# Performance work log

Measured on AMD Instinct MI355X. Metric: run time of the kernel, lower is better.

Reference implementation:

```python
import jax, jax.numpy as jnp
import numpy as np

N_NODES = 100000
IN_F = 128
HID = 64
NUM_CLS = 16
N_EDGES = 1600000
NEG_SLOPE = 0.2


def setup_inputs() -> dict:
    key = jax.random.key(0)
    ks = jax.random.split(key, 10)
    x = jax.random.normal(ks[0], (N_NODES, IN_F), dtype=jnp.float32)
    edge_index = jax.random.randint(ks[1], (2, N_EDGES), 0, N_NODES, dtype=jnp.int64)
    s1 = 1.0 / np.sqrt(IN_F)
    s2 = 1.0 / np.sqrt(HID)
    W1 = jax.random.normal(ks[2], (IN_F, HID), dtype=jnp.float32) * s1
    att_src1 = jax.random.normal(ks[3], (HID,), dtype=jnp.float32) * s2
    att_dst1 = jax.random.normal(ks[4], (HID,), dtype=jnp.float32) * s2
    b1 = jnp.zeros((HID,), dtype=jnp.float32)
    W2 = jax.random.normal(ks[5], (HID, NUM_CLS), dtype=jnp.float32) * s2
    att_src2 = jax.random.normal(ks[6], (NUM_CLS,), dtype=jnp.float32) * 0.25
    att_dst2 = jax.random.normal(ks[7], (NUM_CLS,), dtype=jnp.float32) * 0.25
    b2 = jnp.zeros((NUM_CLS,), dtype=jnp.float32)
    return {"x": x, "edge_index": edge_index, "W1": W1, "att_src1": att_src1,
            "att_dst1": att_dst1, "b1": b1, "W2": W2, "att_src2": att_src2,
            "att_dst2": att_dst2, "b2": b2}


def _gat_conv(x, src, dst, W, a_src, a_dst, b, n_nodes):
    # PyG GATConv, heads=1: h = xW; e_ij = LeakyReLU(a_src.h_j + a_dst.h_i)
    h = x @ W  # [N, D]
    e_s = h @ a_src  # [N]
    e_d = h @ a_dst  # [N]
    e = jax.nn.leaky_relu(e_s[src] + e_d[dst], NEG_SLOPE)  # [E]
    # segment softmax over incoming edges per destination node
    m = jax.ops.segment_max(e, dst, num_segments=n_nodes)  # [N]
    ex = jnp.exp(e - m[dst])
    z = jax.ops.segment_sum(ex, dst, num_segments=n_nodes)  # [N]
    alpha = ex / z[dst]  # [E]
    out = jax.ops.segment_sum(h[src] * alpha[:, None], dst, num_segments=n_nodes)
    return out + b


def reference(x, edge_index, W1, att_src1, att_dst1, b1, W2, att_src2, att_dst2, b2):
    n = x.shape[0]
    # add_self_loops=True (PyG default): guarantees non-empty neighborhoods
    loops = jnp.arange(n, dtype=edge_index.dtype)
    src = jnp.concatenate([edge_index[0], loops])
    dst = jnp.concatenate([edge_index[1], loops])
    h = _gat_conv(x, src, dst, W1, att_src1, att_dst1, b1, n)
    h = jax.nn.relu(h)
    # dropout is identity in eval mode
    out = _gat_conv(h, src, dst, W2, att_src2, att_dst2, b2, n)
    return jax.nn.log_softmax(out, axis=1)
```

## Files before the change

### kernel.cpp

```cpp
#include <hip/hip_runtime.h>

#define NEG_SLOPE 0.2f
#define LOG2E 1.44269504f
#define NBUCK 1024
#define BCAP 2560
#define EPB_MAX 8192
#define DCAP 96

typedef __attribute__((ext_vector_type(8))) short bf16x8;
typedef __attribute__((ext_vector_type(4))) float f32x4;

static __device__ __forceinline__ float lrelu(float x) { return fmaxf(x, NEG_SLOPE * x); }

static __device__ __forceinline__ float b2f(unsigned short u) {
    union { unsigned int i; float f; } c; c.i = ((unsigned int)u) << 16; return c.f;
}
static __device__ __forceinline__ unsigned short f2b(float f) {
    union { float f; unsigned int i; } c; c.f = f;
    unsigned int r = c.i + 0x7fff + ((c.i >> 16) & 1);
    return (unsigned short)(r >> 16);
}


__global__ __launch_bounds__(256) void bucket_place(const int* __restrict__ src, const int* __restrict__ dst,
                                                    unsigned int* __restrict__ gblock, int* __restrict__ blkofs,
                                                    int ne, int epb) {
    __shared__ int cnt[NBUCK];
    __shared__ unsigned int stage[EPB_MAX];
    __shared__ int ws4[4];
    __shared__ int totals;
    int tid = threadIdx.x, lane = tid & 63, wid = tid >> 6;
    int blk = blockIdx.x;
    for (int i = tid; i < NBUCK; i += 256) cnt[i] = 0;
    __syncthreads();
    int lo = blk * epb;
    int hi = min(ne, lo + epb);
    for (int i = lo + tid; i < hi; i += 256) atomicAdd(&cnt[dst[i] >> 7], 1);
    __syncthreads();
    int c0 = cnt[4 * tid + 0], c1 = cnt[4 * tid + 1], c2 = cnt[4 * tid + 2], c3 = cnt[4 * tid + 3];
    int s = c0 + c1 + c2 + c3;
    int incl = s;
    #pragma unroll
    for (int off = 1; off < 64; off <<= 1) {
        int u = __shfl_up(incl, off, 64);
        if (lane >= off) incl += u;
    }
    if (lane == 63) ws4[wid] = incl;
    __syncthreads();
    if (tid < 4) {
        int v = ws4[tid];
        int iv = v;
        #pragma unroll
        for (int off = 1; off < 4; off <<= 1) {
            int u = __shfl_up(iv, off, 64);
            if (tid >= off) iv += u;
        }
        ws4[tid] = iv;
        if (tid == 3) totals = iv;
    }
    __syncthreads();
    int base = incl - s + (wid > 0 ? ws4[wid - 1] : 0);
    long long brow = (long long)blk * (NBUCK + 1);
    int o0 = base, o1 = base + c0, o2 = base + c0 + c1, o3 = base + c0 + c1 + c2;
    blkofs[brow + 4 * tid + 0] = o0;
    blkofs[brow + 4 * tid + 1] = o1;
    blkofs[brow + 4 * tid + 2] = o2;
    blkofs[brow + 4 * tid + 3] = o3;
    __syncthreads();
    cnt[4 * tid + 0] = o0; cnt[4 * tid + 1] = o1;
    cnt[4 * tid + 2] = o2; cnt[4 * tid + 3] = o3;
    if (tid == 255) blkofs[brow + NBUCK] = totals;
    __syncthreads();
    for (int i = lo + tid; i < hi; i += 256) {
        int d = dst[i];
        int p = atomicAdd(&cnt[d >> 7], 1);
        stage[p] = (unsigned int)src[i] | (((unsigned int)(d & 127)) << 17);
    }
    __syncthreads();
    int total = totals;
    for (int i = tid; i < total; i += 256)
        gblock[(size_t)blk * epb + i] = stage[i];
}


__global__ __launch_bounds__(256) void bucket_csr(const unsigned int* __restrict__ gblock,
                                                  const int* __restrict__ blkofs,
                                                  int* __restrict__ rowstart, int* __restrict__ deg,
                                                  int* __restrict__ csrc, int n, int epb) {
    int b = blockIdx.x;
    int nodebase = b << 7;
    if (nodebase >= n) return;
    __shared__ unsigned int stage[BCAP];
    __shared__ int hist[128], cur[128], ws[4];
    __shared__ int totals;
    int tid = threadIdx.x, lane = tid & 63, wid = tid >> 6;
    long long brow = (long long)tid * (NBUCK + 1);
    int r0 = blkofs[brow + b];
    int r1 = blkofs[brow + b + 1];
    int len = r1 - r0;
    int incl = len;
    #pragma unroll
    for (int off = 1; off < 64; off <<= 1) {
        int u = __shfl_up(incl, off, 64);
        if (lane >= off) incl += u;
    }
    if (lane == 63) ws[wid] = incl;
    __syncthreads();
    if (tid < 4) {
        int v = ws[tid];
        int iv = v;
        #pragma unroll
        for (int off = 1; off < 4; off <<= 1) {
            int u = __shfl_up(iv, off, 64);
            if (tid >= off) iv += u;
        }
        ws[tid] = iv;
        if (tid == 3) totals = iv;
    }
    __syncthreads();
    int myofs = incl - len + (wid > 0 ? ws[wid - 1] : 0);
    for (int k = 0; k < len; ++k) {
        int p = myofs + k;
        if (p < BCAP) stage[p] = gblock[(size_t)tid * epb + r0 + k];
    }
    if (tid < 128) hist[tid] = 0;
    __syncthreads();
    int cntb = min(totals, BCAP);
    for (int i = tid; i < cntb; i += 256) atomicAdd(&hist[(stage[i] >> 17) & 127], 1);
    __syncthreads();
    int v = 0, incl2 = 0;
    if (tid < 128) {
        v = hist[tid];
        incl2 = v;
        #pragma unroll
        for (int off = 1; off < 64; off <<= 1) {
            int u = __shfl_up(incl2, off, 64);
            if (lane >= off) incl2 += u;
        }
        if (lane == 63) ws[wid] = incl2;
    }
    __syncthreads();
    if (tid < 128) {
        int excl = incl2 - v + (wid == 1 ? ws[0] : 0);
        int node = nodebase + tid;
        if (node < n) { rowstart[node] = b * BCAP + excl; deg[node] = v; }
        cur[tid] = excl;
    }
    __syncthreads();
    for (int i = tid; i < cntb; i += 256) {
        unsigned int e = stage[i];
        int ld = (e >> 17) & 127;
        int p = atomicAdd(&cur[ld], 1);
        csrc[b * BCAP + p] = (int)(e & 0x1FFFFu);
    }
}


__global__ __launch_bounds__(256) void wprep(const float* __restrict__ W1,
                                             unsigned short* __restrict__ WfH,
                                             unsigned short* __restrict__ WfL) {
    int lane = threadIdx.x & 63, cb = threadIdx.x >> 6;
    int r16 = lane & 15, g4 = lane >> 4;
    for (int kb = 0; kb < 4; ++kb) {
        #pragma unroll
        for (int i = 0; i < 8; ++i) {
            int k = kb * 32 + g4 * 8 + i;
            float v = W1[k * 64 + cb * 16 + r16];
            unsigned short hi = f2b(v);
            unsigned short lo = f2b(v - b2f(hi));
            WfH[((cb * 4 + kb) * 64 + lane) * 8 + i] = hi;
            WfL[((cb * 4 + kb) * 64 + lane) * 8 + i] = lo;
        }
    }
}


__global__ __launch_bounds__(256) void gemm1(const float* __restrict__ x,
                                             const unsigned short* __restrict__ WfH,
                                             const unsigned short* __restrict__ WfL,
                                             const float* __restrict__ asrc, const float* __restrict__ adst,
                                             unsigned short* __restrict__ h, float* __restrict__ es,
                                             float* __restrict__ ed, int n) {
    __shared__ unsigned short AsH[64 * 128];
    __shared__ unsigned short AsL[64 * 128];
    int tid = threadIdx.x, lane = tid & 63, wid = tid >> 6;
    int r16 = lane & 15, g4 = lane >> 4;

    int base = blockIdx.x * 64;
    #pragma unroll
    for (int jj = 0; jj < 8; ++jj) {
        int idx = tid + jj * 256;
        int r = idx >> 5, c4 = idx & 31;
        int nidx = base + r;
        float4 v = make_float4(0.f, 0.f, 0.f, 0.f);
        if (nidx < n) v = *(const float4*)&x[(size_t)nidx * 128 + c4 * 4];
        unsigned short h0 = f2b(v.x), h1_ = f2b(v.y), h2_ = f2b(v.z), h3_ = f2b(v.w);
        unsigned short l0 = f2b(v.x - b2f(h0)), l1 = f2b(v.y - b2f(h1_));
        unsigned short l2 = f2b(v.z - b2f(h2_)), l3 = f2b(v.w - b2f(h3_));
        int u = c4 >> 1;
        int swz = (((u ^ (r & 15)) << 1) | (c4 & 1)) << 2;
        *(unsigned long long*)&AsH[r * 128 + swz] =
            (unsigned long long)h0 | ((unsigned long long)h1_ << 16) |
            ((unsigned long long)h2_ << 32) | ((unsigned long long)h3_ << 48);
        *(unsigned long long*)&AsL[r * 128 + swz] =
            (unsigned long long)l0 | ((unsigned long long)l1 << 16) |
            ((unsigned long long)l2 << 32) | ((unsigned long long)l3 << 48);
    }
    __syncthreads();

    bf16x8 afH[4], afL[4];
    int arow = wid * 16 + r16;
    #pragma unroll
    for (int kb = 0; kb < 4; ++kb) {
        int uu = (kb * 4 + g4) ^ r16;
        afH[kb] = *(const bf16x8*)&AsH[arow * 128 + uu * 8];
        afL[kb] = *(const bf16x8*)&AsL[arow * 128 + uu * 8];
    }

    f32x4 acc[4] = {{0.f,0.f,0.f,0.f},{0.f,0.f,0.f,0.f},{0.f,0.f,0.f,0.f},{0.f,0.f,0.f,0.f}};
    #pragma unroll
    for (int cb = 0; cb < 4; ++cb) {
        #pragma unroll
        for (int kb = 0; kb < 4; ++kb) {
            bf16x8 bH = *(const bf16x8*)&WfH[((cb * 4 + kb) * 64 + lane) * 8];
            bf16x8 bL = *(const bf16x8*)&WfL[((cb * 4 + kb) * 64 + lane) * 8];
            acc[cb] = __builtin_amdgcn_mfma_f32_16x16x32_bf16(afH[kb], bH, acc[cb], 0, 0, 0);
            acc[cb] = __builtin_amdgcn_mfma_f32_16x16x32_bf16(afL[kb], bH, acc[cb], 0, 0, 0);
            acc[cb] = __builtin_amdgcn_mfma_f32_16x16x32_bf16(afH[kb], bL, acc[cb], 0, 0, 0);
        }
    }

    float ps[4] = {0.f,0.f,0.f,0.f}, pd[4] = {0.f,0.f,0.f,0.f};
    #pragma unroll
    for (int cb = 0; cb < 4; ++cb) {
        int col = cb * 16 + r16;
        float av = asrc[col], dv = adst[col];
        #pragma unroll
        for (int rg = 0; rg < 4; ++rg) {
            int nidx = base + wid * 16 + g4 * 4 + rg;
            float v = acc[cb][rg];
            if (nidx < n) h[(size_t)nidx * 64 + col] = f2b(v);
            ps[rg] = fmaf(v, av, ps[rg]);
            pd[rg] = fmaf(v, dv, pd[rg]);
        }
    }
    #pragma unroll
    for (int off = 8; off >= 1; off >>= 1) {
        #pragma unroll
        for (int rg = 0; rg < 4; ++rg) {
            ps[rg] += __shfl_xor(ps[rg], off, 64);
            pd[rg] += __shfl_xor(pd[rg], off, 64);
        }
    }
    if (r16 == 0) {
        #pragma unroll
        for (int rg = 0; rg < 4; ++rg) {
            int nidx = base + wid * 16 + g4 * 4 + rg;
            if (nidx < n) { es[nidx] = ps[rg] * LOG2E; ed[nidx] = pd[rg] * LOG2E; }
        }
    }
}


static __device__ __forceinline__ void prep_phase(const float* __restrict__ es, const float* __restrict__ ed,
                                                  const int* __restrict__ rowstart, const int* __restrict__ deg,
                                                  const int* __restrict__ csrc,
                                                  float2 (*ealds)[DCAP], float* aselfs,
                                                  int node, int ln, int l32) {
    float edn = ed[node];
    float e0 = lrelu(es[node] + edn);
    int s0 = rowstart[node], cnt = min(deg[node], DCAP);
    int padded = (cnt + 7) & ~7;
    if (cnt <= 32) {
        int sl = 0; float e = -3.0e38f;
        if (l32 < cnt) { sl = csrc[s0 + l32]; e = lrelu(es[sl] + edn); }
        float m = fmaxf(e, e0);
        #pragma unroll
        for (int off = 16; off >= 1; off >>= 1) m = fmaxf(m, __shfl_xor(m, off, 64));
        float p = (l32 < cnt) ? __builtin_amdgcn_exp2f(e - m) : 0.f;
        float z = p;
        #pragma unroll
        for (int off = 16; off >= 1; off >>= 1) z += __shfl_xor(z, off, 64);
        float p0 = __builtin_amdgcn_exp2f(e0 - m);
        float zi = 1.f / (z + p0);
        if (l32 < cnt) ealds[ln][l32] = make_float2(__int_as_float(sl), p * zi);
        else if (l32 < padded) ealds[ln][l32] = make_float2(__int_as_float(node), 0.f);
        if (l32 == 0) aselfs[ln] = p0 * zi;
    } else {
        float m = e0;
        for (int c = l32; c < cnt; c += 32)
            m = fmaxf(m, lrelu(es[csrc[s0 + c]] + edn));
        #pragma unroll
        for (int off = 16; off >= 1; off >>= 1) m = fmaxf(m, __shfl_xor(m, off, 64));
        float z = 0.f;
        for (int c = l32; c < cnt; c += 32) {
            int sl = csrc[s0 + c];
            float p = __builtin_amdgcn_exp2f(lrelu(es[sl] + edn) - m);
            ealds[ln][c] = make_float2(__int_as_float(sl), p);
            z += p;
        }
        #pragma unroll
        for (int off = 16; off >= 1; off >>= 1) z += __shfl_xor(z, off, 64);
        float p0 = __builtin_amdgcn_exp2f(e0 - m);
        float zi = 1.f / (z + p0);
        for (int c = l32; c < cnt; c += 32) ealds[ln][c].y *= zi;
        if (l32 < padded - cnt) ealds[ln][cnt + l32] = make_float2(__int_as_float(node), 0.f);
        if (l32 == 0) aselfs[ln] = p0 * zi;
    }
}


__global__ __launch_bounds__(256) void fgather1(const unsigned short* __restrict__ h,
                                                const float* __restrict__ es, const float* __restrict__ ed,
                                                const float* __restrict__ b1,
                                                const int* __restrict__ rowstart, const int* __restrict__ deg,
                                                const int* __restrict__ csrc,
                                                unsigned short* __restrict__ out, int n) {
    __shared__ float2 ealds[8][DCAP];
    __shared__ float aselfs[8];
    int wid = threadIdx.x >> 6, lane = threadIdx.x & 63;
    int half = lane >> 5, l32 = lane & 31;
    int nbase = blockIdx.x * 8;
    int pnode = nbase + wid * 2 + half;
    if (pnode < n)
        prep_phase(es, ed, rowstart, deg, csrc, ealds, aselfs, pnode, wid * 2 + half, l32);
    __syncthreads();

    int sg = lane >> 4, q = lane & 15;
    for (int t = 0; t < 2; ++t) {
        int node = nbase + wid * 2 + t;
        if (node >= n) break;
        int ln = wid * 2 + t;
        float a0_, a1_, a2_, a3_;
        {
            ushort4 hv = *(const ushort4*)&h[(unsigned)(node * 64) + q * 4];
            float a = (sg == 0) ? aselfs[ln] : 0.f;
            a0_ = a * b2f(hv.x); a1_ = a * b2f(hv.y);
            a2_ = a * b2f(hv.z); a3_ = a * b2f(hv.w);
        }
        int cnt = min(deg[node], DCAP);
        int iters = (cnt + 3) >> 2;
        int j = 0;
        for (; j + 4 <= iters; j += 4) {
            float2 tA = ealds[ln][(j + 0) * 4 + sg];
            float2 tB = ealds[ln][(j + 1) * 4 + sg];
            float2 tC = ealds[ln][(j + 2) * 4 + sg];
            float2 tD = ealds[ln][(j + 3) * 4 + sg];
            int sA = __float_as_int(tA.x), sB = __float_as_int(tB.x);
            int sC = __float_as_int(tC.x), sD = __float_as_int(tD.x);
            ushort4 hA = *(const ushort4*)&h[(unsigned)(sA * 64) + q * 4];
            ushort4 hB = *(const ushort4*)&h[(unsigned)(sB * 64) + q * 4];
            ushort4 hC = *(const ushort4*)&h[(unsigned)(sC * 64) + q * 4];
            ushort4 hD = *(const ushort4*)&h[(unsigned)(sD * 64) + q * 4];
            a0_ = fmaf(b2f(hA.x), tA.y, a0_); a1_ = fmaf(b2f(hA.y), tA.y, a1_);
            a2_ = fmaf(b2f(hA.z), tA.y, a2_); a3_ = fmaf(b2f(hA.w), tA.y, a3_);
            a0_ = fmaf(b2f(hB.x), tB.y, a0_); a1_ = fmaf(b2f(hB.y), tB.y, a1_);
            a2_ = fmaf(b2f(hB.z), tB.y, a2_); a3_ = fmaf(b2f(hB.w), tB.y, a3_);
            a0_ = fmaf(b2f(hC.x), tC.y, a0_); a1_ = fmaf(b2f(hC.y), tC.y, a1_);
            a2_ = fmaf(b2f(hC.z), tC.y, a2_); a3_ = fmaf(b2f(hC.w), tC.y, a3_);
            a0_ = fmaf(b2f(hD.x), tD.y, a0_); a1_ = fmaf(b2f(hD.y), tD.y, a1_);
            a2_ = fmaf(b2f(hD.z), tD.y, a2_); a3_ = fmaf(b2f(hD.w), tD.y, a3_);
        }
        for (; j < iters; ++j) {
            float2 tE = ealds[ln][j * 4 + sg];
            int s = __float_as_int(tE.x);
            ushort4 hv = *(const ushort4*)&h[(unsigned)(s * 64) + q * 4];
            a0_ = fmaf(b2f(hv.x), tE.y, a0_); a1_ = fmaf(b2f(hv.y), tE.y, a1_);
            a2_ = fmaf(b2f(hv.z), tE.y, a2_); a3_ = fmaf(b2f(hv.w), tE.y, a3_);
        }
        #pragma unroll
        for (int off = 16; off <= 32; off <<= 1) {
            a0_ += __shfl_xor(a0_, off, 64);
            a1_ += __shfl_xor(a1_, off, 64);
            a2_ += __shfl_xor(a2_, off, 64);
            a3_ += __shfl_xor(a3_, off, 64);
        }
        if (sg == 0) {
            float o0 = a0_ + b1[q * 4 + 0], o1 = a1_ + b1[q * 4 + 1];
            float o2 = a2_ + b1[q * 4 + 2], o3 = a3_ + b1[q * 4 + 3];
            ushort4 pk;
            pk.x = f2b(o0 > 0.f ? o0 : 0.f); pk.y = f2b(o1 > 0.f ? o1 : 0.f);
            pk.z = f2b(o2 > 0.f ? o2 : 0.f); pk.w = f2b(o3 > 0.f ? o3 : 0.f);
            *(ushort4*)&out[(unsigned)(node * 64) + q * 4] = pk;
        }
    }
}


__global__ __launch_bounds__(256) void gemm2(const unsigned short* __restrict__ hin, const float* __restrict__ W2,
                                             const float* __restrict__ asrc, const float* __restrict__ adst,
                                             unsigned short* __restrict__ h2, float* __restrict__ es,
                                             float* __restrict__ ed, int n) {
    __shared__ float xl[16][64];
    int tid = threadIdx.x;
    int lane = tid & 63, wid = tid >> 6;
    int sub = lane >> 4, j = lane & 15;
    float w2[64];
    #pragma unroll
    for (int k = 0; k < 64; ++k) w2[k] = W2[k * 16 + j];
    int base = blockIdx.x * 16;
    for (int i = tid; i < 16 * 64; i += 256) {
        int r = i >> 6, c = i & 63;
        int nidx = base + r;
        xl[r][c] = (nidx < n) ? b2f(hin[(unsigned)(nidx * 64) + c]) : 0.f;
    }
    __syncthreads();
    int r = wid * 4 + sub;
    int nidx = base + r;
    if (nidx < n) {
        float acc = 0.f;
        #pragma unroll
        for (int kk = 0; kk < 16; ++kk) {
            float4 xv = *(const float4*)&xl[r][kk * 4];
            acc = fmaf(xv.x, w2[4 * kk + 0], acc);
            acc = fmaf(xv.y, w2[4 * kk + 1], acc);
            acc = fmaf(xv.z, w2[4 * kk + 2], acc);
            acc = fmaf(xv.w, w2[4 * kk + 3], acc);
        }
        h2[(unsigned)(nidx * 16) + j] = f2b(acc);
        float s = acc * asrc[j], d = acc * adst[j];
        #pragma unroll
        for (int off = 8; off >= 1; off >>= 1) {
            s += __shfl_xor(s, off, 64);
            d += __shfl_xor(d, off, 64);
        }
        if (j == 0) { es[nidx] = s * LOG2E; ed[nidx] = d * LOG2E; }
    }
}


__global__ __launch_bounds__(256) void fgather2(const unsigned short* __restrict__ h,
                                                const float* __restrict__ es, const float* __restrict__ ed,
                                                const float* __restrict__ b2,
                                                const int* __restrict__ rowstart, const int* __restrict__ deg,
                                                const int* __restrict__ csrc,
                                                float* __restrict__ out, int n) {
    __shared__ float2 ealds[8][DCAP];
    __shared__ float aselfs[8];
    int wid = threadIdx.x >> 6, lane = threadIdx.x & 63;
    int half = lane >> 5, l32 = lane & 31;
    int nbase = blockIdx.x * 8;
    int pnode = nbase + wid * 2 + half;
    if (pnode < n)
        prep_phase(es, ed, rowstart, deg, csrc, ealds, aselfs, pnode, wid * 2 + half, l32);
    __syncthreads();

    int sg = lane >> 3, p = lane & 7;
    for (int t = 0; t < 2; ++t) {
        int node = nbase + wid * 2 + t;
        if (node >= n) break;
        int ln = wid * 2 + t;
        float a0_, a1_;
        {
            ushort2 hv = *(const ushort2*)&h[(unsigned)(node * 16) + p * 2];
            float a = (sg == 0) ? aselfs[ln] : 0.f;
            a0_ = a * b2f(hv.x); a1_ = a * b2f(hv.y);
        }
        int cnt = min(deg[node], DCAP);
        int iters = (cnt + 7) >> 3;
        int j = 0;
        for (; j + 2 <= iters; j += 2) {
            float2 tA = ealds[ln][(j + 0) * 8 + sg];
            float2 tB = ealds[ln][(j + 1) * 8 + sg];
            int sA = __float_as_int(tA.x), sB = __float_as_int(tB.x);
            ushort2 hA = *(const ushort2*)&h[(unsigned)(sA * 16) + p * 2];
            ushort2 hB = *(const ushort2*)&h[(unsigned)(sB * 16) + p * 2];
            a0_ = fmaf(b2f(hA.x), tA.y, a0_); a1_ = fmaf(b2f(hA.y), tA.y, a1_);
            a0_ = fmaf(b2f(hB.x), tB.y, a0_); a1_ = fmaf(b2f(hB.y), tB.y, a1_);
        }
        for (; j < iters; ++j) {
            float2 tE = ealds[ln][j * 8 + sg];
            int s = __float_as_int(tE.x);
            ushort2 hv = *(const ushort2*)&h[(unsigned)(s * 16) + p * 2];
            a0_ = fmaf(b2f(hv.x), tE.y, a0_); a1_ = fmaf(b2f(hv.y), tE.y, a1_);
        }
        #pragma unroll
        for (int off = 8; off <= 32; off <<= 1) {
            a0_ += __shfl_xor(a0_, off, 64);
            a1_ += __shfl_xor(a1_, off, 64);
        }
        float v0 = a0_ + b2[p * 2 + 0];
        float v1 = a1_ + b2[p * 2 + 1];
        float mx = fmaxf(v0, v1);
        #pragma unroll
        for (int off = 4; off >= 1; off >>= 1) mx = fmaxf(mx, __shfl_xor(mx, off, 64));
        float se = __expf(v0 - mx) + __expf(v1 - mx);
        #pragma unroll
        for (int off = 4; off >= 1; off >>= 1) se += __shfl_xor(se, off, 64);
        float ls = __logf(se);
        if (sg == 0) {
            float2 res = make_float2(v0 - mx - ls, v1 - mx - ls);
            *(float2*)&out[(unsigned)(node * 16) + p * 2] = res;
        }
    }
}


extern "C" void kernel_launch(void* const* d_in, const int* in_sizes, int n_in,
                              void* d_out, int out_size, void* d_ws, size_t ws_size,
                              hipStream_t stream) {
    const float* x   = (const float*)d_in[0];
    const int*   ei  = (const int*)d_in[1];
    const float* W1  = (const float*)d_in[2];
    const float* as1 = (const float*)d_in[3];
    const float* ad1 = (const float*)d_in[4];
    const float* b1  = (const float*)d_in[5];
    const float* W2  = (const float*)d_in[6];
    const float* as2 = (const float*)d_in[7];
    const float* ad2 = (const float*)d_in[8];
    const float* b2  = (const float*)d_in[9];
    int n  = in_sizes[0] / 128;
    int ne = in_sizes[1] / 2;
    const int* srcv = ei;
    const int* dstv = ei + ne;

    char* ws = (char*)d_ws;
    size_t off = 0;
    auto alloc = [&](size_t bytes) -> void* {
        void* p = ws + off;
        off = (off + bytes + 255) & ~(size_t)255;
        return p;
    };
    unsigned short* h1 = (unsigned short*)alloc((size_t)n * 64 * 2);
    unsigned short* hr = (unsigned short*)alloc((size_t)n * 64 * 2);
    unsigned short* h2 = (unsigned short*)alloc((size_t)n * 16 * 2);
    float* es1  = (float*)alloc((size_t)n * 4);
    float* ed1  = (float*)alloc((size_t)n * 4);
    float* es2  = (float*)alloc((size_t)n * 4);
    float* ed2  = (float*)alloc((size_t)n * 4);
    unsigned short* WfH = (unsigned short*)alloc(16 * 64 * 8 * 2);
    unsigned short* WfL = (unsigned short*)alloc(16 * 64 * 8 * 2);
    int* deg      = (int*)alloc((size_t)n * 4);
    int* rowstart = (int*)alloc((size_t)n * 4);
    int nblk = 256;
    int epb = (ne + nblk - 1) / nblk;
    unsigned int* gblock = (unsigned int*)alloc((size_t)nblk * epb * 4);
    int* blkofs   = (int*)alloc((size_t)nblk * (NBUCK + 1) * 4);
    int* csrc     = (int*)alloc((size_t)NBUCK * BCAP * 4);

    bucket_place<<<nblk, 256, 0, stream>>>(srcv, dstv, gblock, blkofs, ne, epb);
    bucket_csr<<<NBUCK, 256, 0, stream>>>(gblock, blkofs, rowstart, deg, csrc, n, epb);

    wprep<<<1, 256, 0, stream>>>(W1, WfH, WfL);
    gemm1<<<(n + 63) / 64, 256, 0, stream>>>(x, WfH, WfL, as1, ad1, h1, es1, ed1, n);
    fgather1<<<(n + 7) / 8, 256, 0, stream>>>(h1, es1, ed1, b1, rowstart, deg, csrc, hr, n);

    gemm2<<<(n + 15) / 16, 256, 0, stream>>>(hr, W2, as2, ad2, h2, es2, ed2, n);
    fgather2<<<(n + 7) / 8, 256, 0, stream>>>(h2, es2, ed2, b2, rowstart, deg, csrc, (float*)d_out, n);
}
```

Measured before the change: 170.0 us.

## Merge bucket placement and first GEMM into one heterogeneous launch

```diff
diff --git a/kernel.cpp b/kernel.cpp
--- a/kernel.cpp
+++ b/kernel.cpp
@@ -22,64 +22,156 @@
 }
 
 
-__global__ __launch_bounds__(256) void bucket_place(const int* __restrict__ src, const int* __restrict__ dst,
-                                                    unsigned int* __restrict__ gblock, int* __restrict__ blkofs,
-                                                    int ne, int epb) {
-    __shared__ int cnt[NBUCK];
-    __shared__ unsigned int stage[EPB_MAX];
+__global__ __launch_bounds__(256) void k1(const int* __restrict__ src, const int* __restrict__ dst,
+                                          unsigned int* __restrict__ gblock, int* __restrict__ blkofs,
+                                          int ne, int epb, int nplace,
+                                          const float* __restrict__ x, const float* __restrict__ W1,
+                                          const float* __restrict__ asrc, const float* __restrict__ adst,
+                                          unsigned short* __restrict__ h, float* __restrict__ es,
+                                          float* __restrict__ ed, int n) {
+    __shared__ __align__(16) char smem[4096 + EPB_MAX * 4];
     __shared__ int ws4[4];
     __shared__ int totals;
     int tid = threadIdx.x, lane = tid & 63, wid = tid >> 6;
-    int blk = blockIdx.x;
-    for (int i = tid; i < NBUCK; i += 256) cnt[i] = 0;
-    __syncthreads();
-    int lo = blk * epb;
-    int hi = min(ne, lo + epb);
-    for (int i = lo + tid; i < hi; i += 256) atomicAdd(&cnt[dst[i] >> 7], 1);
-    __syncthreads();
-    int c0 = cnt[4 * tid + 0], c1 = cnt[4 * tid + 1], c2 = cnt[4 * tid + 2], c3 = cnt[4 * tid + 3];
-    int s = c0 + c1 + c2 + c3;
-    int incl = s;
-    #pragma unroll
-    for (int off = 1; off < 64; off <<= 1) {
-        int u = __shfl_up(incl, off, 64);
-        if (lane >= off) incl += u;
-    }
-    if (lane == 63) ws4[wid] = incl;
-    __syncthreads();
-    if (tid < 4) {
-        int v = ws4[tid];
-        int iv = v;
-        #pragma unroll
-        for (int off = 1; off < 4; off <<= 1) {
-            int u = __shfl_up(iv, off, 64);
-            if (tid >= off) iv += u;
-        }
-        ws4[tid] = iv;
-        if (tid == 3) totals = iv;
-    }
-    __syncthreads();
-    int base = incl - s + (wid > 0 ? ws4[wid - 1] : 0);
-    long long brow = (long long)blk * (NBUCK + 1);
-    int o0 = base, o1 = base + c0, o2 = base + c0 + c1, o3 = base + c0 + c1 + c2;
-    blkofs[brow + 4 * tid + 0] = o0;
-    blkofs[brow + 4 * tid + 1] = o1;
-    blkofs[brow + 4 * tid + 2] = o2;
-    blkofs[brow + 4 * tid + 3] = o3;
-    __syncthreads();
-    cnt[4 * tid + 0] = o0; cnt[4 * tid + 1] = o1;
-    cnt[4 * tid + 2] = o2; cnt[4 * tid + 3] = o3;
-    if (tid == 255) blkofs[brow + NBUCK] = totals;
-    __syncthreads();
-    for (int i = lo + tid; i < hi; i += 256) {
-        int d = dst[i];
-        int p = atomicAdd(&cnt[d >> 7], 1);
-        stage[p] = (unsigned int)src[i] | (((unsigned int)(d & 127)) << 17);
-    }
-    __syncthreads();
-    int total = totals;
-    for (int i = tid; i < total; i += 256)
-        gblock[(size_t)blk * epb + i] = stage[i];
+
+    if (blockIdx.x < (unsigned)nplace) {
+        int* cnt = (int*)smem;
+        unsigned int* stage = (unsigned int*)(smem + 4096);
+        int blk = blockIdx.x;
+        for (int i = tid; i < NBUCK; i += 256) cnt[i] = 0;
+        __syncthreads();
+        int lo = blk * epb;
+        int hi = min(ne, lo + epb);
+        for (int i = lo + tid; i < hi; i += 256) atomicAdd(&cnt[dst[i] >> 7], 1);
+        __syncthreads();
+        int c0 = cnt[4 * tid + 0], c1 = cnt[4 * tid + 1], c2 = cnt[4 * tid + 2], c3 = cnt[4 * tid + 3];
+        int s = c0 + c1 + c2 + c3;
+        int incl = s;
+        #pragma unroll
+        for (int off = 1; off < 64; off <<= 1) {
+            int u = __shfl_up(incl, off, 64);
+            if (lane >= off) incl += u;
+        }
+        if (lane == 63) ws4[wid] = incl;
+        __syncthreads();
+        if (tid < 4) {
+            int v = ws4[tid];
+            int iv = v;
+            #pragma unroll
+            for (int off = 1; off < 4; off <<= 1) {
+                int u = __shfl_up(iv, off, 64);
+                if (tid >= off) iv += u;
+            }
+            ws4[tid] = iv;
+            if (tid == 3) totals = iv;
+        }
+        __syncthreads();
+        int base = incl - s + (wid > 0 ? ws4[wid - 1] : 0);
+        long long brow = (long long)blk * (NBUCK + 1);
+        int o0 = base, o1 = base + c0, o2 = base + c0 + c1, o3 = base + c0 + c1 + c2;
+        blkofs[brow + 4 * tid + 0] = o0;
+        blkofs[brow + 4 * tid + 1] = o1;
+        blkofs[brow + 4 * tid + 2] = o2;
+        blkofs[brow + 4 * tid + 3] = o3;
+        __syncthreads();
+        cnt[4 * tid + 0] = o0; cnt[4 * tid + 1] = o1;
+        cnt[4 * tid + 2] = o2; cnt[4 * tid + 3] = o3;
+        if (tid == 255) blkofs[brow + NBUCK] = totals;
+        __syncthreads();
+        for (int i = lo + tid; i < hi; i += 256) {
+            int d = dst[i];
+            int p = atomicAdd(&cnt[d >> 7], 1);
+            stage[p] = (unsigned int)src[i] | (((unsigned int)(d & 127)) << 17);
+        }
+        __syncthreads();
+        int total = totals;
+        for (int i = tid; i < total; i += 256)
+            gblock[(size_t)blk * epb + i] = stage[i];
+    } else {
+        unsigned short* AsH = (unsigned short*)smem;
+        unsigned short* AsL = (unsigned short*)(smem + 16384);
+        int r16 = lane & 15, g4 = lane >> 4;
+        int base = (blockIdx.x - nplace) * 64;
+        #pragma unroll
+        for (int jj = 0; jj < 8; ++jj) {
+            int idx = tid + jj * 256;
+            int r = idx >> 5, c4 = idx & 31;
+            int nidx = base + r;
+            float4 v = make_float4(0.f, 0.f, 0.f, 0.f);
+            if (nidx < n) v = *(const float4*)&x[(size_t)nidx * 128 + c4 * 4];
+            unsigned short h0 = f2b(v.x), h1_ = f2b(v.y), h2_ = f2b(v.z), h3_ = f2b(v.w);
+            unsigned short l0 = f2b(v.x - b2f(h0)), l1 = f2b(v.y - b2f(h1_));
+            unsigned short l2 = f2b(v.z - b2f(h2_)), l3 = f2b(v.w - b2f(h3_));
+            int u = c4 >> 1;
+            int swz = (((u ^ (r & 15)) << 1) | (c4 & 1)) << 2;
+            *(unsigned long long*)&AsH[r * 128 + swz] =
+                (unsigned long long)h0 | ((unsigned long long)h1_ << 16) |
+                ((unsigned long long)h2_ << 32) | ((unsigned long long)h3_ << 48);
+            *(unsigned long long*)&AsL[r * 128 + swz] =
+                (unsigned long long)l0 | ((unsigned long long)l1 << 16) |
+                ((unsigned long long)l2 << 32) | ((unsigned long long)l3 << 48);
+        }
+        __syncthreads();
+
+        bf16x8 afH[4], afL[4];
+        int arow = wid * 16 + r16;
+        #pragma unroll
+        for (int kb = 0; kb < 4; ++kb) {
+            int uu = (kb * 4 + g4) ^ r16;
+            afH[kb] = *(const bf16x8*)&AsH[arow * 128 + uu * 8];
+            afL[kb] = *(const bf16x8*)&AsL[arow * 128 + uu * 8];
+        }
+
+        f32x4 acc[4] = {{0.f,0.f,0.f,0.f},{0.f,0.f,0.f,0.f},{0.f,0.f,0.f,0.f},{0.f,0.f,0.f,0.f}};
+        #pragma unroll
+        for (int cb = 0; cb < 4; ++cb) {
+            #pragma unroll
+            for (int kb = 0; kb < 4; ++kb) {
+                union { bf16x8 v; unsigned short u[8]; } bH, bL;
+                #pragma unroll
+                for (int i = 0; i < 8; ++i) {
+                    int k = kb * 32 + g4 * 8 + i;
+                    float w = W1[k * 64 + cb * 16 + r16];
+                    unsigned short hi = f2b(w);
+                    bH.u[i] = hi;
+                    bL.u[i] = f2b(w - b2f(hi));
+                }
+                acc[cb] = __builtin_amdgcn_mfma_f32_16x16x32_bf16(afH[kb], bH.v, acc[cb], 0, 0, 0);
+                acc[cb] = __builtin_amdgcn_mfma_f32_16x16x32_bf16(afL[kb], bH.v, acc[cb], 0, 0, 0);
+                acc[cb] = __builtin_amdgcn_mfma_f32_16x16x32_bf16(afH[kb], bL.v, acc[cb], 0, 0, 0);
+            }
+        }
+
+        float ps[4] = {0.f,0.f,0.f,0.f}, pd[4] = {0.f,0.f,0.f,0.f};
+        #pragma unroll
+        for (int cb = 0; cb < 4; ++cb) {
+            int col = cb * 16 + r16;
+            float av = asrc[col], dv = adst[col];
+            #pragma unroll
+            for (int rg = 0; rg < 4; ++rg) {
+                int nidx = base + wid * 16 + g4 * 4 + rg;
+                float v = acc[cb][rg];
+                if (nidx < n) h[(size_t)nidx * 64 + col] = f2b(v);
+                ps[rg] = fmaf(v, av, ps[rg]);
+                pd[rg] = fmaf(v, dv, pd[rg]);
+            }
+        }
+        #pragma unroll
+        for (int off = 8; off >= 1; off >>= 1) {
+            #pragma unroll
+            for (int rg = 0; rg < 4; ++rg) {
+                ps[rg] += __shfl_xor(ps[rg], off, 64);
+                pd[rg] += __shfl_xor(pd[rg], off, 64);
+            }
+        }
+        if (r16 == 0) {
+            #pragma unroll
+            for (int rg = 0; rg < 4; ++rg) {
+                int nidx = base + wid * 16 + g4 * 4 + rg;
+                if (nidx < n) { es[nidx] = ps[rg] * LOG2E; ed[nidx] = pd[rg] * LOG2E; }
+            }
+        }
+    }
 }
 
 
@@ -152,112 +244,6 @@
         int ld = (e >> 17) & 127;
         int p = atomicAdd(&cur[ld], 1);
         csrc[b * BCAP + p] = (int)(e & 0x1FFFFu);
-    }
-}
-
-
-__global__ __launch_bounds__(256) void wprep(const float* __restrict__ W1,
-                                             unsigned short* __restrict__ WfH,
-                                             unsigned short* __restrict__ WfL) {
-    int lane = threadIdx.x & 63, cb = threadIdx.x >> 6;
-    int r16 = lane & 15, g4 = lane >> 4;
-    for (int kb = 0; kb < 4; ++kb) {
-        #pragma unroll
-        for (int i = 0; i < 8; ++i) {
-            int k = kb * 32 + g4 * 8 + i;
-            float v = W1[k * 64 + cb * 16 + r16];
-            unsigned short hi = f2b(v);
-            unsigned short lo = f2b(v - b2f(hi));
-            WfH[((cb * 4 + kb) * 64 + lane) * 8 + i] = hi;
-            WfL[((cb * 4 + kb) * 64 + lane) * 8 + i] = lo;
-        }
-    }
-}
-
-
-__global__ __launch_bounds__(256) void gemm1(const float* __restrict__ x,
-                                             const unsigned short* __restrict__ WfH,
-                                             const unsigned short* __restrict__ WfL,
-                                             const float* __restrict__ asrc, const float* __restrict__ adst,
-                                             unsigned short* __restrict__ h, float* __restrict__ es,
-                                             float* __restrict__ ed, int n) {
-    __shared__ unsigned short AsH[64 * 128];
-    __shared__ unsigned short AsL[64 * 128];
-    int tid = threadIdx.x, lane = tid & 63, wid = tid >> 6;
-    int r16 = lane & 15, g4 = lane >> 4;
-
-    int base = blockIdx.x * 64;
-    #pragma unroll
-    for (int jj = 0; jj < 8; ++jj) {
-        int idx = tid + jj * 256;
-        int r = idx >> 5, c4 = idx & 31;
-        int nidx = base + r;
-        float4 v = make_float4(0.f, 0.f, 0.f, 0.f);
-        if (nidx < n) v = *(const float4*)&x[(size_t)nidx * 128 + c4 * 4];
-        unsigned short h0 = f2b(v.x), h1_ = f2b(v.y), h2_ = f2b(v.z), h3_ = f2b(v.w);
-        unsigned short l0 = f2b(v.x - b2f(h0)), l1 = f2b(v.y - b2f(h1_));
-        unsigned short l2 = f2b(v.z - b2f(h2_)), l3 = f2b(v.w - b2f(h3_));
-        int u = c4 >> 1;
-        int swz = (((u ^ (r & 15)) << 1) | (c4 & 1)) << 2;
-        *(unsigned long long*)&AsH[r * 128 + swz] =
-            (unsigned long long)h0 | ((unsigned long long)h1_ << 16) |
-            ((unsigned long long)h2_ << 32) | ((unsigned long long)h3_ << 48);
-        *(unsigned long long*)&AsL[r * 128 + swz] =
-            (unsigned long long)l0 | ((unsigned long long)l1 << 16) |
-            ((unsigned long long)l2 << 32) | ((unsigned long long)l3 << 48);
-    }
-    __syncthreads();
-
-    bf16x8 afH[4], afL[4];
-    int arow = wid * 16 + r16;
-    #pragma unroll
-    for (int kb = 0; kb < 4; ++kb) {
-        int uu = (kb * 4 + g4) ^ r16;
-        afH[kb] = *(const bf16x8*)&AsH[arow * 128 + uu * 8];
-        afL[kb] = *(const bf16x8*)&AsL[arow * 128 + uu * 8];
-    }
-
-    f32x4 acc[4] = {{0.f,0.f,0.f,0.f},{0.f,0.f,0.f,0.f},{0.f,0.f,0.f,0.f},{0.f,0.f,0.f,0.f}};
-    #pragma unroll
-    for (int cb = 0; cb < 4; ++cb) {
-        #pragma unroll
-        for (int kb = 0; kb < 4; ++kb) {
-            bf16x8 bH = *(const bf16x8*)&WfH[((cb * 4 + kb) * 64 + lane) * 8];
-            bf16x8 bL = *(const bf16x8*)&WfL[((cb * 4 + kb) * 64 + lane) * 8];
-            acc[cb] = __builtin_amdgcn_mfma_f32_16x16x32_bf16(afH[kb], bH, acc[cb], 0, 0, 0);
-            acc[cb] = __builtin_amdgcn_mfma_f32_16x16x32_bf16(afL[kb], bH, acc[cb], 0, 0, 0);
-            acc[cb] = __builtin_amdgcn_mfma_f32_16x16x32_bf16(afH[kb], bL, acc[cb], 0, 0, 0);
-        }
-    }
-
-    float ps[4] = {0.f,0.f,0.f,0.f}, pd[4] = {0.f,0.f,0.f,0.f};
-    #pragma unroll
-    for (int cb = 0; cb < 4; ++cb) {
-        int col = cb * 16 + r16;
-        float av = asrc[col], dv = adst[col];
-        #pragma unroll
-        for (int rg = 0; rg < 4; ++rg) {
-            int nidx = base + wid * 16 + g4 * 4 + rg;
-            float v = acc[cb][rg];
-            if (nidx < n) h[(size_t)nidx * 64 + col] = f2b(v);
-            ps[rg] = fmaf(v, av, ps[rg]);
-            pd[rg] = fmaf(v, dv, pd[rg]);
-        }
-    }
-    #pragma unroll
-    for (int off = 8; off >= 1; off >>= 1) {
-        #pragma unroll
-        for (int rg = 0; rg < 4; ++rg) {
-            ps[rg] += __shfl_xor(ps[rg], off, 64);
-            pd[rg] += __shfl_xor(pd[rg], off, 64);
-        }
-    }
-    if (r16 == 0) {
-        #pragma unroll
-        for (int rg = 0; rg < 4; ++rg) {
-            int nidx = base + wid * 16 + g4 * 4 + rg;
-            if (nidx < n) { es[nidx] = ps[rg] * LOG2E; ed[nidx] = pd[rg] * LOG2E; }
-        }
     }
 }
 
@@ -528,23 +514,19 @@
     float* ed1  = (float*)alloc((size_t)n * 4);
     float* es2  = (float*)alloc((size_t)n * 4);
     float* ed2  = (float*)alloc((size_t)n * 4);
-    unsigned short* WfH = (unsigned short*)alloc(16 * 64 * 8 * 2);
-    unsigned short* WfL = (unsigned short*)alloc(16 * 64 * 8 * 2);
     int* deg      = (int*)alloc((size_t)n * 4);
     int* rowstart = (int*)alloc((size_t)n * 4);
-    int nblk = 256;
-    int epb = (ne + nblk - 1) / nblk;
-    unsigned int* gblock = (unsigned int*)alloc((size_t)nblk * epb * 4);
-    int* blkofs   = (int*)alloc((size_t)nblk * (NBUCK + 1) * 4);
+    int nplace = 256;
+    int epb = (ne + nplace - 1) / nplace;
+    unsigned int* gblock = (unsigned int*)alloc((size_t)nplace * epb * 4);
+    int* blkofs   = (int*)alloc((size_t)nplace * (NBUCK + 1) * 4);
     int* csrc     = (int*)alloc((size_t)NBUCK * BCAP * 4);
 
-    bucket_place<<<nblk, 256, 0, stream>>>(srcv, dstv, gblock, blkofs, ne, epb);
+    int ngemm = (n + 63) / 64;
+    k1<<<nplace + ngemm, 256, 0, stream>>>(srcv, dstv, gblock, blkofs, ne, epb, nplace,
+                                           x, W1, as1, ad1, h1, es1, ed1, n);
     bucket_csr<<<NBUCK, 256, 0, stream>>>(gblock, blkofs, rowstart, deg, csrc, n, epb);
-
-    wprep<<<1, 256, 0, stream>>>(W1, WfH, WfL);
-    gemm1<<<(n + 63) / 64, 256, 0, stream>>>(x, WfH, WfL, as1, ad1, h1, es1, ed1, n);
     fgather1<<<(n + 7) / 8, 256, 0, stream>>>(h1, es1, ed1, b1, rowstart, deg, csrc, hr, n);
-
     gemm2<<<(n + 15) / 16, 256, 0, stream>>>(hr, W2, as2, ad2, h2, es2, ed2, n);
     fgather2<<<(n + 7) / 8, 256, 0, stream>>>(h2, es2, ed2, b2, rowstart, deg, csrc, (float*)d_out, n);
 }
```

New measurement: 149.4 us, median of 3. -12.2%, faster.

## Merge bucket placement and first GEMM into one launch for concurrent execution

Applied to the files above, without the earlier changes.

```diff
diff --git a/kernel.cpp b/kernel.cpp
--- a/kernel.cpp
+++ b/kernel.cpp
@@ -22,64 +22,170 @@
 }
 
 
-__global__ __launch_bounds__(256) void bucket_place(const int* __restrict__ src, const int* __restrict__ dst,
-                                                    unsigned int* __restrict__ gblock, int* __restrict__ blkofs,
-                                                    int ne, int epb) {
-    __shared__ int cnt[NBUCK];
-    __shared__ unsigned int stage[EPB_MAX];
+__global__ __launch_bounds__(256) void wprep(const float* __restrict__ W1,
+                                             unsigned short* __restrict__ WfH,
+                                             unsigned short* __restrict__ WfL) {
+    int lane = threadIdx.x & 63, cb = threadIdx.x >> 6;
+    int r16 = lane & 15, g4 = lane >> 4;
+    for (int kb = 0; kb < 4; ++kb) {
+        #pragma unroll
+        for (int i = 0; i < 8; ++i) {
+            int k = kb * 32 + g4 * 8 + i;
+            float v = W1[k * 64 + cb * 16 + r16];
+            unsigned short hi = f2b(v);
+            unsigned short lo = f2b(v - b2f(hi));
+            WfH[((cb * 4 + kb) * 64 + lane) * 8 + i] = hi;
+            WfL[((cb * 4 + kb) * 64 + lane) * 8 + i] = lo;
+        }
+    }
+}
+
+
+__global__ __launch_bounds__(256) void k1(const int* __restrict__ src, const int* __restrict__ dst,
+                                          unsigned int* __restrict__ gblock, int* __restrict__ blkofs,
+                                          int ne, int epb, int nplace,
+                                          const float* __restrict__ x,
+                                          const unsigned short* __restrict__ WfH,
+                                          const unsigned short* __restrict__ WfL,
+                                          const float* __restrict__ asrc, const float* __restrict__ adst,
+                                          unsigned short* __restrict__ h, float* __restrict__ es,
+                                          float* __restrict__ ed, int n) {
+    __shared__ __align__(16) char smem[4096 + EPB_MAX * 4];
     __shared__ int ws4[4];
     __shared__ int totals;
     int tid = threadIdx.x, lane = tid & 63, wid = tid >> 6;
-    int blk = blockIdx.x;
-    for (int i = tid; i < NBUCK; i += 256) cnt[i] = 0;
-    __syncthreads();
-    int lo = blk * epb;
-    int hi = min(ne, lo + epb);
-    for (int i = lo + tid; i < hi; i += 256) atomicAdd(&cnt[dst[i] >> 7], 1);
-    __syncthreads();
-    int c0 = cnt[4 * tid + 0], c1 = cnt[4 * tid + 1], c2 = cnt[4 * tid + 2], c3 = cnt[4 * tid + 3];
-    int s = c0 + c1 + c2 + c3;
-    int incl = s;
-    #pragma unroll
-    for (int off = 1; off < 64; off <<= 1) {
-        int u = __shfl_up(incl, off, 64);
-        if (lane >= off) incl += u;
-    }
-    if (lane == 63) ws4[wid] = incl;
-    __syncthreads();
-    if (tid < 4) {
-        int v = ws4[tid];
-        int iv = v;
-        #pragma unroll
-        for (int off = 1; off < 4; off <<= 1) {
-            int u = __shfl_up(iv, off, 64);
-            if (tid >= off) iv += u;
-        }
-        ws4[tid] = iv;
-        if (tid == 3) totals = iv;
-    }
-    __syncthreads();
-    int base = incl - s + (wid > 0 ? ws4[wid - 1] : 0);
-    long long brow = (long long)blk * (NBUCK + 1);
-    int o0 = base, o1 = base + c0, o2 = base + c0 + c1, o3 = base + c0 + c1 + c2;
-    blkofs[brow + 4 * tid + 0] = o0;
-    blkofs[brow + 4 * tid + 1] = o1;
-    blkofs[brow + 4 * tid + 2] = o2;
-    blkofs[brow + 4 * tid + 3] = o3;
-    __syncthreads();
-    cnt[4 * tid + 0] = o0; cnt[4 * tid + 1] = o1;
-    cnt[4 * tid + 2] = o2; cnt[4 * tid + 3] = o3;
-    if (tid == 255) blkofs[brow + NBUCK] = totals;
-    __syncthreads();
-    for (int i = lo + tid; i < hi; i += 256) {
-        int d = dst[i];
-        int p = atomicAdd(&cnt[d >> 7], 1);
-        stage[p] = (unsigned int)src[i] | (((unsigned int)(d & 127)) << 17);
-    }
-    __syncthreads();
-    int total = totals;
-    for (int i = tid; i < total; i += 256)
-        gblock[(size_t)blk * epb + i] = stage[i];
+
+    if (blockIdx.x < (unsigned)nplace) {
+        int* cnt = (int*)smem;
+        unsigned int* stage = (unsigned int*)(smem + 4096);
+        int blk = blockIdx.x;
+        for (int i = tid; i < NBUCK; i += 256) cnt[i] = 0;
+        __syncthreads();
+        int lo = blk * epb;
+        int hi = min(ne, lo + epb);
+        for (int i = lo + tid; i < hi; i += 256) atomicAdd(&cnt[dst[i] >> 7], 1);
+        __syncthreads();
+        int c0 = cnt[4 * tid + 0], c1 = cnt[4 * tid + 1], c2 = cnt[4 * tid + 2], c3 = cnt[4 * tid + 3];
+        int s = c0 + c1 + c2 + c3;
+        int incl = s;
+        #pragma unroll
+        for (int off = 1; off < 64; off <<= 1) {
+            int u = __shfl_up(incl, off, 64);
+            if (lane >= off) incl += u;
+        }
+        if (lane == 63) ws4[wid] = incl;
+        __syncthreads();
+        if (tid < 4) {
+            int v = ws4[tid];
+            int iv = v;
+            #pragma unroll
+            for (int off = 1; off < 4; off <<= 1) {
+                int u = __shfl_up(iv, off, 64);
+                if (tid >= off) iv += u;
+            }
+            ws4[tid] = iv;
+            if (tid == 3) totals = iv;
+        }
+        __syncthreads();
+        int base = incl - s + (wid > 0 ? ws4[wid - 1] : 0);
+        long long brow = (long long)blk * (NBUCK + 1);
+        int o0 = base, o1 = base + c0, o2 = base + c0 + c1, o3 = base + c0 + c1 + c2;
+        blkofs[brow + 4 * tid + 0] = o0;
+        blkofs[brow + 4 * tid + 1] = o1;
+        blkofs[brow + 4 * tid + 2] = o2;
+        blkofs[brow + 4 * tid + 3] = o3;
+        __syncthreads();
+        cnt[4 * tid + 0] = o0; cnt[4 * tid + 1] = o1;
+        cnt[4 * tid + 2] = o2; cnt[4 * tid + 3] = o3;
+        if (tid == 255) blkofs[brow + NBUCK] = totals;
+        __syncthreads();
+        for (int i = lo + tid; i < hi; i += 256) {
+            int d = dst[i];
+            int p = atomicAdd(&cnt[d >> 7], 1);
+            stage[p] = (unsigned int)src[i] | (((unsigned int)(d & 127)) << 17);
+        }
+        __syncthreads();
+        int total = totals;
+        for (int i = tid; i < total; i += 256)
+            gblock[(size_t)blk * epb + i] = stage[i];
+    } else {
+        unsigned short* AsH = (unsigned short*)smem;
+        unsigned short* AsL = (unsigned short*)(smem + 16384);
+        int r16 = lane & 15, g4 = lane >> 4;
+        int base = (blockIdx.x - nplace) * 64;
+        #pragma unroll
+        for (int jj = 0; jj < 8; ++jj) {
+            int idx = tid + jj * 256;
+            int r = idx >> 5, c4 = idx & 31;
+            int nidx = base + r;
+            float4 v = make_float4(0.f, 0.f, 0.f, 0.f);
+            if (nidx < n) v = *(const float4*)&x[(size_t)nidx * 128 + c4 * 4];
+            unsigned short h0 = f2b(v.x), h1_ = f2b(v.y), h2_ = f2b(v.z), h3_ = f2b(v.w);
+            unsigned short l0 = f2b(v.x - b2f(h0)), l1 = f2b(v.y - b2f(h1_));
+            unsigned short l2 = f2b(v.z - b2f(h2_)), l3 = f2b(v.w - b2f(h3_));
+            int u = c4 >> 1;
+            int swz = (((u ^ (r & 15)) << 1) | (c4 & 1)) << 2;
+            *(unsigned long long*)&AsH[r * 128 + swz] =
+                (unsigned long long)h0 | ((unsigned long long)h1_ << 16) |
+                ((unsigned long long)h2_ << 32) | ((unsigned long long)h3_ << 48);
+            *(unsigned long long*)&AsL[r * 128 + swz] =
+                (unsigned long long)l0 | ((unsigned long long)l1 << 16) |
+                ((unsigned long long)l2 << 32) | ((unsigned long long)l3 << 48);
+        }
+        __syncthreads();
+
+        bf16x8 afH[4], afL[4];
+        int arow = wid * 16 + r16;
+        #pragma unroll
+        for (int kb = 0; kb < 4; ++kb) {
+            int uu = (kb * 4 + g4) ^ r16;
+            afH[kb] = *(const bf16x8*)&AsH[arow * 128 + uu * 8];
+            afL[kb] = *(const bf16x8*)&AsL[arow * 128 + uu * 8];
+        }
+
+        f32x4 acc[4] = {{0.f,0.f,0.f,0.f},{0.f,0.f,0.f,0.f},{0.f,0.f,0.f,0.f},{0.f,0.f,0.f,0.f}};
+        #pragma unroll
+        for (int cb = 0; cb < 4; ++cb) {
+            #pragma unroll
+            for (int kb = 0; kb < 4; ++kb) {
+                bf16x8 bH = *(const bf16x8*)&WfH[((cb * 4 + kb) * 64 + lane) * 8];
+                bf16x8 bL = *(const bf16x8*)&WfL[((cb * 4 + kb) * 64 + lane) * 8];
+                acc[cb] = __builtin_amdgcn_mfma_f32_16x16x32_bf16(afH[kb], bH, acc[cb], 0, 0, 0);
+                acc[cb] = __builtin_amdgcn_mfma_f32_16x16x32_bf16(afL[kb], bH, acc[cb], 0, 0, 0);
+                acc[cb] = __builtin_amdgcn_mfma_f32_16x16x32_bf16(afH[kb], bL, acc[cb], 0, 0, 0);
+            }
+        }
+
+        float ps[4] = {0.f,0.f,0.f,0.f}, pd[4] = {0.f,0.f,0.f,0.f};
+        #pragma unroll
+        for (int cb = 0; cb < 4; ++cb) {
+            int col = cb * 16 + r16;
+            float av = asrc[col], dv = adst[col];
+            #pragma unroll
+            for (int rg = 0; rg < 4; ++rg) {
+                int nidx = base + wid * 16 + g4 * 4 + rg;
+                float v = acc[cb][rg];
+                if (nidx < n) h[(size_t)nidx * 64 + col] = f2b(v);
+                ps[rg] = fmaf(v, av, ps[rg]);
+                pd[rg] = fmaf(v, dv, pd[rg]);
+            }
+        }
+        #pragma unroll
+        for (int off = 8; off >= 1; off >>= 1) {
+            #pragma unroll
+            for (int rg = 0; rg < 4; ++rg) {
+                ps[rg] += __shfl_xor(ps[rg], off, 64);
+                pd[rg] += __shfl_xor(pd[rg], off, 64);
+            }
+        }
+        if (r16 == 0) {
+            #pragma unroll
+            for (int rg = 0; rg < 4; ++rg) {
+                int nidx = base + wid * 16 + g4 * 4 + rg;
+                if (nidx < n) { es[nidx] = ps[rg] * LOG2E; ed[nidx] = pd[rg] * LOG2E; }
+            }
+        }
+    }
 }
 
 
@@ -152,112 +258,6 @@
         int ld = (e >> 17) & 127;
         int p = atomicAdd(&cur[ld], 1);
         csrc[b * BCAP + p] = (int)(e & 0x1FFFFu);
-    }
-}
-
-
-__global__ __launch_bounds__(256) void wprep(const float* __restrict__ W1,
-                                             unsigned short* __restrict__ WfH,
-                                             unsigned short* __restrict__ WfL) {
-    int lane = threadIdx.x & 63, cb = threadIdx.x >> 6;
-    int r16 = lane & 15, g4 = lane >> 4;
-    for (int kb = 0; kb < 4; ++kb) {
-        #pragma unroll
-        for (int i = 0; i < 8; ++i) {
-            int k = kb * 32 + g4 * 8 + i;
-            float v = W1[k * 64 + cb * 16 + r16];
-            unsigned short hi = f2b(v);
-            unsigned short lo = f2b(v - b2f(hi));
-            WfH[((cb * 4 + kb) * 64 + lane) * 8 + i] = hi;
-            WfL[((cb * 4 + kb) * 64 + lane) * 8 + i] = lo;
-        }
-    }
-}
-
-
-__global__ __launch_bounds__(256) void gemm1(const float* __restrict__ x,
-                                             const unsigned short* __restrict__ WfH,
-                                             const unsigned short* __restrict__ WfL,
-                                             const float* __restrict__ asrc, const float* __restrict__ adst,
-                                             unsigned short* __restrict__ h, float* __restrict__ es,
-                                             float* __restrict__ ed, int n) {
-    __shared__ unsigned short AsH[64 * 128];
-    __shared__ unsigned short AsL[64 * 128];
-    int tid = threadIdx.x, lane = tid & 63, wid = tid >> 6;
-    int r16 = lane & 15, g4 = lane >> 4;
-
-    int base = blockIdx.x * 64;
-    #pragma unroll
-    for (int jj = 0; jj < 8; ++jj) {
-        int idx = tid + jj * 256;
-        int r = idx >> 5, c4 = idx & 31;
-        int nidx = base + r;
-        float4 v = make_float4(0.f, 0.f, 0.f, 0.f);
-        if (nidx < n) v = *(const float4*)&x[(size_t)nidx * 128 + c4 * 4];
-        unsigned short h0 = f2b(v.x), h1_ = f2b(v.y), h2_ = f2b(v.z), h3_ = f2b(v.w);
-        unsigned short l0 = f2b(v.x - b2f(h0)), l1 = f2b(v.y - b2f(h1_));
-        unsigned short l2 = f2b(v.z - b2f(h2_)), l3 = f2b(v.w - b2f(h3_));
-        int u = c4 >> 1;
-        int swz = (((u ^ (r & 15)) << 1) | (c4 & 1)) << 2;
-        *(unsigned long long*)&AsH[r * 128 + swz] =
-            (unsigned long long)h0 | ((unsigned long long)h1_ << 16) |
-            ((unsigned long long)h2_ << 32) | ((unsigned long long)h3_ << 48);
-        *(unsigned long long*)&AsL[r * 128 + swz] =
-            (unsigned long long)l0 | ((unsigned long long)l1 << 16) |
-            ((unsigned long long)l2 << 32) | ((unsigned long long)l3 << 48);
-    }
-    __syncthreads();
-
-    bf16x8 afH[4], afL[4];
-    int arow = wid * 16 + r16;
-    #pragma unroll
-    for (int kb = 0; kb < 4; ++kb) {
-        int uu = (kb * 4 + g4) ^ r16;
-        afH[kb] = *(const bf16x8*)&AsH[arow * 128 + uu * 8];
-        afL[kb] = *(const bf16x8*)&AsL[arow * 128 + uu * 8];
-    }
-
-    f32x4 acc[4] = {{0.f,0.f,0.f,0.f},{0.f,0.f,0.f,0.f},{0.f,0.f,0.f,0.f},{0.f,0.f,0.f,0.f}};
-    #pragma unroll
-    for (int cb = 0; cb < 4; ++cb) {
-        #pragma unroll
-        for (int kb = 0; kb < 4; ++kb) {
-            bf16x8 bH = *(const bf16x8*)&WfH[((cb * 4 + kb) * 64 + lane) * 8];
-            bf16x8 bL = *(const bf16x8*)&WfL[((cb * 4 + kb) * 64 + lane) * 8];
-            acc[cb] = __builtin_amdgcn_mfma_f32_16x16x32_bf16(afH[kb], bH, acc[cb], 0, 0, 0);
-            acc[cb] = __builtin_amdgcn_mfma_f32_16x16x32_bf16(afL[kb], bH, acc[cb], 0, 0, 0);
-            acc[cb] = __builtin_amdgcn_mfma_f32_16x16x32_bf16(afH[kb], bL, acc[cb], 0, 0, 0);
-        }
-    }
-
-    float ps[4] = {0.f,0.f,0.f,0.f}, pd[4] = {0.f,0.f,0.f,0.f};
-    #pragma unroll
-    for (int cb = 0; cb < 4; ++cb) {
-        int col = cb * 16 + r16;
-        float av = asrc[col], dv = adst[col];
-        #pragma unroll
-        for (int rg = 0; rg < 4; ++rg) {
-            int nidx = base + wid * 16 + g4 * 4 + rg;
-            float v = acc[cb][rg];
-            if (nidx < n) h[(size_t)nidx * 64 + col] = f2b(v);
-            ps[rg] = fmaf(v, av, ps[rg]);
-            pd[rg] = fmaf(v, dv, pd[rg]);
-        }
-    }
-    #pragma unroll
-    for (int off = 8; off >= 1; off >>= 1) {
-        #pragma unroll
-        for (int rg = 0; rg < 4; ++rg) {
-            ps[rg] += __shfl_xor(ps[rg], off, 64);
-            pd[rg] += __shfl_xor(pd[rg], off, 64);
-        }
-    }
-    if (r16 == 0) {
-        #pragma unroll
-        for (int rg = 0; rg < 4; ++rg) {
-            int nidx = base + wid * 16 + g4 * 4 + rg;
-            if (nidx < n) { es[nidx] = ps[rg] * LOG2E; ed[nidx] = pd[rg] * LOG2E; }
-        }
     }
 }
 
@@ -532,19 +532,18 @@
     unsigned short* WfL = (unsigned short*)alloc(16 * 64 * 8 * 2);
     int* deg      = (int*)alloc((size_t)n * 4);
     int* rowstart = (int*)alloc((size_t)n * 4);
-    int nblk = 256;
-    int epb = (ne + nblk - 1) / nblk;
-    unsigned int* gblock = (unsigned int*)alloc((size_t)nblk * epb * 4);
-    int* blkofs   = (int*)alloc((size_t)nblk * (NBUCK + 1) * 4);
+    int nplace = 256;
+    int epb = (ne + nplace - 1) / nplace;
+    unsigned int* gblock = (unsigned int*)alloc((size_t)nplace * epb * 4);
+    int* blkofs   = (int*)alloc((size_t)nplace * (NBUCK + 1) * 4);
     int* csrc     = (int*)alloc((size_t)NBUCK * BCAP * 4);
 
-    bucket_place<<<nblk, 256, 0, stream>>>(srcv, dstv, gblock, blkofs, ne, epb);
+    int ngemm = (n + 63) / 64;
+    wprep<<<1, 256, 0, stream>>>(W1, WfH, WfL);
+    k1<<<nplace + ngemm, 256, 0, stream>>>(srcv, dstv, gblock, blkofs, ne, epb, nplace,
+                                           x, WfH, WfL, as1, ad1, h1, es1, ed1, n);
     bucket_csr<<<NBUCK, 256, 0, stream>>>(gblock, blkofs, rowstart, deg, csrc, n, epb);
-
-    wprep<<<1, 256, 0, stream>>>(W1, WfH, WfL);
-    gemm1<<<(n + 63) / 64, 256, 0, stream>>>(x, WfH, WfL, as1, ad1, h1, es1, ed1, n);
     fgather1<<<(n + 7) / 8, 256, 0, stream>>>(h1, es1, ed1, b1, rowstart, deg, csrc, hr, n);
-
     gemm2<<<(n + 15) / 16, 256, 0, stream>>>(hr, W2, as2, ad2, h2, es2, ed2, n);
     fgather2<<<(n + 7) / 8, 256, 0, stream>>>(h2, es2, ed2, b2, rowstart, deg, csrc, (float*)d_out, n);
 }
```

Result: faster. 156.3 us (-8.1%).
